# Optimization experiments

Measured on AMD Instinct MI355X. Metric: run time of the kernel, lower is better.

## Reference

```python
import jax, jax.numpy as jnp
import numpy as np

EPS = 1e-12

def setup_inputs() -> dict:
    key = jax.random.key(0)
    k1, k2, k3, k4, k5, k6 = jax.random.split(key, 6)
    B, DIM, T = 16, 256, 2048
    K, D = 1024, 64  # num_embeddings, embedding_dim
    N = B * T
    input_data = jax.random.normal(k1, (B, DIM, T), dtype=jnp.float32)
    codebooks = jax.random.normal(k2, (K, D), dtype=jnp.float32)
    W_in = jax.random.normal(k3, (DIM, D), dtype=jnp.float32) / np.sqrt(DIM)
    b_in = jnp.zeros((D,), dtype=jnp.float32)
    W_out = jax.random.normal(k4, (D, DIM), dtype=jnp.float32) / np.sqrt(D)
    b_out = jnp.zeros((DIM,), dtype=jnp.float32)
    random_vector = jax.random.normal(k5, (N, D), dtype=jnp.float32)
    return {"input_data": input_data, "codebooks": codebooks,
            "W_in": W_in, "b_in": b_in, "W_out": W_out, "b_out": b_out,
            "random_vector": random_vector}

def reference(input_data, codebooks, W_in, b_in, W_out, b_out, random_vector):
    B, DIM, T = input_data.shape
    D = codebooks.shape[1]
    # encode: [B, DIM, T] -> [B, T, DIM] -> project -> [B*T, D]
    x = jnp.einsum('bct,cd->btd', input_data, W_in) + b_in
    x = x.reshape(-1, D)  # [N, D]
    distances = (jnp.sum(x * x, axis=1, keepdims=True)
                 - 2.0 * (x @ codebooks.T)
                 + jnp.sum(codebooks * codebooks, axis=1)[None, :])  # [N, K]
    min_indices = jnp.argmin(distances, axis=1)  # [N]
    hard = codebooks[min_indices]  # [N, D]
    # noise substitution
    norm_resid = jnp.sqrt(jnp.sum((x - hard) ** 2, axis=1, keepdims=True))
    norm_rand = jnp.sqrt(jnp.sum(random_vector ** 2, axis=1, keepdims=True))
    vq_error = (norm_resid / (norm_rand + EPS)) * random_vector
    q = x + vq_error  # [N, D]
    # decode: [N, D] -> [B, T, D] -> project_out -> [B, DIM, T]
    q = q.reshape(B, T, D)
    out = jnp.einsum('btd,dc->bct', q, W_out) + b_out[None, :, None]
    return out
```

## Files before the change

kernel.cpp:

```cpp
#include <hip/hip_runtime.h>
#include <hip/hip_bf16.h>

typedef __bf16 bf16x8 __attribute__((ext_vector_type(8)));
typedef unsigned short u16x8 __attribute__((ext_vector_type(8)));
typedef unsigned int u32x2 __attribute__((ext_vector_type(2)));
typedef float f32x4 __attribute__((ext_vector_type(4)));
typedef unsigned short u16;

constexpr int DIMc = 256, Tt = 2048, Dd = 64;

#define CBF_U  0
#define CN_U   65536
#define WINT_U 67584
#define WOX_U  83968

__device__ __forceinline__ u16 f2b(float f) {
  unsigned u = __float_as_uint(f);
  return (u16)((u + 0x7FFFu + ((u >> 16) & 1u)) >> 16);
}
__device__ __forceinline__ float b2f(u16 v) {
  return __uint_as_float(((unsigned)v) << 16);
}
__device__ __forceinline__ unsigned f2b2(float a, float b) {
  return (unsigned)f2b(a) | ((unsigned)f2b(b) << 16);
}
__device__ __forceinline__ f32x4 mfma16(u16x8 a, u16x8 b, f32x4 c) {
  return __builtin_amdgcn_mfma_f32_16x16x32_bf16(
      __builtin_bit_cast(bf16x8, a), __builtin_bit_cast(bf16x8, b), c, 0, 0, 0);
}
__device__ __forceinline__ void dma16(const u16* g, u16* l) {
  __builtin_amdgcn_global_load_lds(
      (const __attribute__((address_space(1))) unsigned int*)g,
      (__attribute__((address_space(3))) unsigned int*)l, 16, 0, 0);
}

__global__ void nsvq_prep(const float* __restrict__ cb, const float* __restrict__ Win,
                          const float* __restrict__ Wout, u16* __restrict__ wsu) {
  const int g = blockIdx.x * 256 + threadIdx.x;
  {
    const int k = g >> 4, j = (g & 15) << 2;
    float4 v = *(const float4*)(cb + k * 64 + j);
    u16* row = wsu + CBF_U + k * 64 + j;
    row[0] = f2b(-2.f * v.x); row[1] = f2b(-2.f * v.y);
    row[2] = f2b(-2.f * v.z); row[3] = f2b(-2.f * v.w);
  }
  if (g < 1024) {
    const float* cr = cb + g * 64;
    float p[4];
    #pragma unroll
    for (int q = 0; q < 4; ++q) {
      float4 a0 = ((const float4*)(cr + q * 8))[0],      a1 = ((const float4*)(cr + q * 8))[1];
      float4 a2 = ((const float4*)(cr + 32 + q * 8))[0], a3 = ((const float4*)(cr + 32 + q * 8))[1];
      float pA = fmaf(a0.w, a0.w, fmaf(a0.z, a0.z, fmaf(a0.y, a0.y, a0.x * a0.x)));
      float pB = fmaf(a1.w, a1.w, fmaf(a1.z, a1.z, fmaf(a1.y, a1.y, a1.x * a1.x)));
      float pC = fmaf(a2.w, a2.w, fmaf(a2.z, a2.z, fmaf(a2.y, a2.y, a2.x * a2.x)));
      float pD = fmaf(a3.w, a3.w, fmaf(a3.z, a3.z, fmaf(a3.y, a3.y, a3.x * a3.x)));
      p[q] = (pA + pB) + (pC + pD);
    }
    ((float*)(wsu + CN_U))[g] = (p[0] + p[1]) + (p[2] + p[3]);
  }
  {
    const int d = g >> 8, c = g & 255;
    wsu[WINT_U + d * 256 + (((c >> 3) ^ (d & 7)) << 3) + (c & 7)] = f2b(Win[c * 64 + d]);
  }
  {
    const int c = g >> 6, d = g & 63;
    wsu[WOX_U + c * 64 + (((d >> 3) ^ (c & 7)) << 3) + (d & 7)] = f2b(Wout[d * 256 + c]);
  }
}

__global__ __launch_bounds__(256, 2) void nsvq_main(
    const float* __restrict__ in, const float* __restrict__ rnd,
    const float* __restrict__ bin, const float* __restrict__ bout,
    const u16* __restrict__ wsu, float* __restrict__ out) {
  __shared__ u16 sm[37376];
  u16* const WinT = sm;
  u16* const WoX  = sm + 16384;
  u16* const Xt   = sm + 32768;
  float* const mnp = (float*)(sm + 36864);

  const int tid  = threadIdx.x;
  const int lane = tid & 63;
  const int w    = tid >> 6;
  const int quad = lane >> 4, col = lane & 15;
  const int b    = blockIdx.x >> 5;
  const int t0   = (blockIdx.x & 31) << 6;
  const int myt  = w * 16 + col;

  #pragma unroll
  for (int ii = 0; ii < 8; ++ii) {
    const int i = w + 4 * ii;
    dma16(wsu + WINT_U + i * 512 + lane * 8, WinT + i * 512);
  }
  #pragma unroll
  for (int ii = 0; ii < 8; ++ii) {
    const int i = w + 4 * ii;
    dma16(wsu + WOX_U + i * 512 + lane * 8, WoX + i * 512);
  }
  u16x8 Bf[8];
  const float* ibase = in + (size_t)b * DIMc * Tt + t0 + myt;
  #pragma unroll
  for (int kt = 0; kt < 8; ++kt) {
    float v[8];
    #pragma unroll
    for (int j = 0; j < 8; ++j) v[j] = ibase[(size_t)(kt * 32 + quad * 8 + j) * Tt];
    u16x8 pk;
    #pragma unroll
    for (int j = 0; j < 8; ++j) pk[j] = f2b(v[j]);
    Bf[kt] = pk;
  }
  float4 rq[4];
  {
    const float* rbase = rnd + ((size_t)b * Tt + t0 + myt) * Dd + quad * 4;
    #pragma unroll
    for (int mt = 0; mt < 4; ++mt) rq[mt] = *(const float4*)(rbase + mt * 16);
  }
  float rr2v = 0.f;
  #pragma unroll
  for (int mt = 0; mt < 4; ++mt) {
    rr2v = fmaf(rq[mt].x, rq[mt].x, rr2v); rr2v = fmaf(rq[mt].y, rq[mt].y, rr2v);
    rr2v = fmaf(rq[mt].z, rq[mt].z, rr2v); rr2v = fmaf(rq[mt].w, rq[mt].w, rr2v);
  }
  rr2v += __shfl_xor(rr2v, 16);
  rr2v += __shfl_xor(rr2v, 32);
  __syncthreads();

  f32x4 acc[4];
  #pragma unroll
  for (int mt = 0; mt < 4; ++mt) {
    float4 bi = *(const float4*)(bin + mt * 16 + quad * 4);
    f32x4 a = {bi.x, bi.y, bi.z, bi.w};
    const int d = mt * 16 + col;
    #pragma unroll
    for (int kt = 0; kt < 8; ++kt) {
      u16x8 A = *(const u16x8*)(WinT + d * 256 + (((kt * 4 + quad) ^ (d & 7)) << 3));
      a = mfma16(A, Bf[kt], a);
    }
    acc[mt] = a;
  }
  float x2v = 0.f;
  #pragma unroll
  for (int mt = 0; mt < 4; ++mt) {
    #pragma unroll
    for (int r = 0; r < 4; ++r) x2v = fmaf(acc[mt][r], acc[mt][r], x2v);
    u32x2 px = { f2b2(acc[mt][0], acc[mt][1]), f2b2(acc[mt][2], acc[mt][3]) };
    const int bk  = mt * 2 + (quad >> 1);
    const int off = myt * 64 + ((bk ^ (myt & 7)) << 3) + (quad & 1) * 4;
    *(u32x2*)(Xt + off) = px;
  }
  x2v += __shfl_xor(x2v, 16);
  x2v += __shfl_xor(x2v, 32);
  __syncthreads();

  u16x8 Xa[4], Xb[4];
  #pragma unroll
  for (int nt = 0; nt < 4; ++nt) {
    const int tr = nt * 16 + col;
    Xa[nt] = *(const u16x8*)(Xt + tr * 64 + ((quad ^ (tr & 7)) << 3));
    Xb[nt] = *(const u16x8*)(Xt + tr * 64 + (((4 + quad) ^ (tr & 7)) << 3));
  }
  float minv[4];
  #pragma unroll
  for (int i = 0; i < 4; ++i) minv[i] = 3.4e38f;
  const u16* cwf   = wsu + CBF_U + (size_t)(w * 256) * 64;
  const float* cnp = (const float*)(wsu + CN_U) + w * 256;
  #pragma unroll 4
  for (int mi = 0; mi < 16; ++mi) {
    u16x8 A0 = *(const u16x8*)(cwf + (mi * 16 + col) * 64 + quad * 8);
    u16x8 A1 = *(const u16x8*)(cwf + (mi * 16 + col) * 64 + 32 + quad * 8);
    f32x4 cn4 = *(const f32x4*)(cnp + mi * 16 + quad * 4);
    #pragma unroll
    for (int nt = 0; nt < 4; ++nt) {
      f32x4 a = mfma16(A0, Xa[nt], cn4);
      a = mfma16(A1, Xb[nt], a);
      #pragma unroll
      for (int r = 0; r < 4; ++r) minv[nt] = fminf(minv[nt], a[r]);
    }
  }
  #pragma unroll
  for (int nt = 0; nt < 4; ++nt) {
    float m = minv[nt];
    m = fminf(m, __shfl_xor(m, 16));
    m = fminf(m, __shfl_xor(m, 32));
    mnp[w * 64 + nt * 16 + col] = m;
  }
  __syncthreads();

  float mv = 3.4e38f;
  #pragma unroll
  for (int j = 0; j < 4; ++j) mv = fminf(mv, mnp[j * 64 + myt]);
  float r2  = fmaxf(x2v + mv, 0.f);
  float scv = sqrtf(r2) / (sqrtf(rr2v) + 1e-12f);
  #pragma unroll
  for (int mt = 0; mt < 4; ++mt) {
    float q0 = fmaf(scv, rq[mt].x, acc[mt][0]);
    float q1 = fmaf(scv, rq[mt].y, acc[mt][1]);
    float q2 = fmaf(scv, rq[mt].z, acc[mt][2]);
    float q3 = fmaf(scv, rq[mt].w, acc[mt][3]);
    u32x2 pq = { f2b2(q0, q1), f2b2(q2, q3) };
    const int bk  = mt * 2 + (quad >> 1);
    const int off = myt * 64 + ((bk ^ (myt & 7)) << 3) + (quad & 1) * 4;
    *(u32x2*)(Xt + off) = pq;
  }

  u16x8 Q0 = *(const u16x8*)(Xt + myt * 64 + ((quad ^ (myt & 7)) << 3));
  u16x8 Q1 = *(const u16x8*)(Xt + myt * 64 + (((4 + quad) ^ (myt & 7)) << 3));
  float* ob0 = out + (size_t)b * DIMc * Tt + t0 + myt;
  #pragma unroll
  for (int mt = 0; mt < 16; ++mt) {
    const int c = mt * 16 + col;
    const u16* ar = WoX + c * 64;
    u16x8 A0 = *(const u16x8*)(ar + ((quad ^ (c & 7)) << 3));
    u16x8 A1 = *(const u16x8*)(ar + (((4 + quad) ^ (c & 7)) << 3));
    float4 bo = *(const float4*)(bout + mt * 16 + quad * 4);
    f32x4 a = {bo.x, bo.y, bo.z, bo.w};
    a = mfma16(A0, Q0, a);
    a = mfma16(A1, Q1, a);
    float* ob = ob0 + (size_t)(mt * 16 + quad * 4) * Tt;
    #pragma unroll
    for (int r = 0; r < 4; ++r) ob[(size_t)r * Tt] = a[r];
  }
}

extern "C" void kernel_launch(void* const* d_in, const int* in_sizes, int n_in,
                              void* d_out, int out_size, void* d_ws, size_t ws_size,
                              hipStream_t stream) {
  const float *in = nullptr, *cbp = nullptr, *rnd = nullptr, *bin = nullptr, *bout = nullptr;
  const float* w16[2] = {nullptr, nullptr}; int nw = 0;
  for (int i = 0; i < n_in; ++i) {
    switch (in_sizes[i]) {
      case 8388608: in  = (const float*)d_in[i]; break;
      case 65536:   cbp = (const float*)d_in[i]; break;
      case 2097152: rnd = (const float*)d_in[i]; break;
      case 64:      bin = (const float*)d_in[i]; break;
      case 256:     bout= (const float*)d_in[i]; break;
      case 16384:   if (nw < 2) w16[nw++] = (const float*)d_in[i]; break;
      default: break;
    }
  }
  if (!in)   in  = (const float*)d_in[0];
  if (!cbp)  cbp = (const float*)d_in[1];
  if (nw < 2) { w16[0] = (const float*)d_in[2]; w16[1] = (const float*)d_in[4]; }
  if (!bin)  bin = (const float*)d_in[3];
  if (!bout) bout = (const float*)d_in[5];
  if (!rnd)  rnd = (const float*)d_in[6];

  u16* wsu = (u16*)d_ws;
  nsvq_prep<<<64, 256, 0, stream>>>(cbp, w16[0], w16[1], wsu);
  nsvq_main<<<512, 256, 0, stream>>>(in, rnd, bin, bout, wsu, (float*)d_out);
}
```

Before: 113.0 us.

## Shrink blocks to 32 tokens, read weights from global, drop LDS weight staging

Each block now handles 32 tokens with 2 waves (1024 blocks of 128 threads) instead of 64 tokens with 4 waves. The W_in and W_out tiles are no longer copied into LDS; MFMA operands are read directly from global/L2 in an unswizzled layout. The random vector is reloaded instead of held in registers. This cuts LDS use and register pressure to allow more resident waves, at the cost of more global/L2 traffic for weights and codebook per token and twice the codebook scan per wave.

After: 132.5 us. 1.17x slower.

```diff
diff --git a/kernel.cpp b/kernel.cpp
--- a/kernel.cpp
+++ b/kernel.cpp
@@ -27,11 +27,6 @@
 __device__ __forceinline__ f32x4 mfma16(u16x8 a, u16x8 b, f32x4 c) {
   return __builtin_amdgcn_mfma_f32_16x16x32_bf16(
       __builtin_bit_cast(bf16x8, a), __builtin_bit_cast(bf16x8, b), c, 0, 0, 0);
-}
-__device__ __forceinline__ void dma16(const u16* g, u16* l) {
-  __builtin_amdgcn_global_load_lds(
-      (const __attribute__((address_space(1))) unsigned int*)g,
-      (__attribute__((address_space(3))) unsigned int*)l, 16, 0, 0);
 }
 
 __global__ void nsvq_prep(const float* __restrict__ cb, const float* __restrict__ Win,
@@ -61,42 +56,30 @@
   }
   {
     const int d = g >> 8, c = g & 255;
-    wsu[WINT_U + d * 256 + (((c >> 3) ^ (d & 7)) << 3) + (c & 7)] = f2b(Win[c * 64 + d]);
+    wsu[WINT_U + d * 256 + c] = f2b(Win[c * 64 + d]);
   }
   {
     const int c = g >> 6, d = g & 63;
-    wsu[WOX_U + c * 64 + (((d >> 3) ^ (c & 7)) << 3) + (d & 7)] = f2b(Wout[d * 256 + c]);
-  }
-}
-
-__global__ __launch_bounds__(256, 2) void nsvq_main(
+    wsu[WOX_U + c * 64 + d] = f2b(Wout[d * 256 + c]);
+  }
+}
+
+__global__ __launch_bounds__(128, 5) void nsvq_main(
     const float* __restrict__ in, const float* __restrict__ rnd,
     const float* __restrict__ bin, const float* __restrict__ bout,
     const u16* __restrict__ wsu, float* __restrict__ out) {
-  __shared__ u16 sm[37376];
-  u16* const WinT = sm;
-  u16* const WoX  = sm + 16384;
-  u16* const Xt   = sm + 32768;
-  float* const mnp = (float*)(sm + 36864);
+  __shared__ u16 sm[2176];
+  u16* const Xt   = sm;
+  float* const mnp = (float*)(sm + 2048);
 
   const int tid  = threadIdx.x;
   const int lane = tid & 63;
   const int w    = tid >> 6;
   const int quad = lane >> 4, col = lane & 15;
-  const int b    = blockIdx.x >> 5;
-  const int t0   = (blockIdx.x & 31) << 6;
+  const int b    = blockIdx.x >> 6;
+  const int t0   = (blockIdx.x & 63) << 5;
   const int myt  = w * 16 + col;
 
-  #pragma unroll
-  for (int ii = 0; ii < 8; ++ii) {
-    const int i = w + 4 * ii;
-    dma16(wsu + WINT_U + i * 512 + lane * 8, WinT + i * 512);
-  }
-  #pragma unroll
-  for (int ii = 0; ii < 8; ++ii) {
-    const int i = w + 4 * ii;
-    dma16(wsu + WOX_U + i * 512 + lane * 8, WoX + i * 512);
-  }
   u16x8 Bf[8];
   const float* ibase = in + (size_t)b * DIMc * Tt + t0 + myt;
   #pragma unroll
@@ -109,22 +92,18 @@
     for (int j = 0; j < 8; ++j) pk[j] = f2b(v[j]);
     Bf[kt] = pk;
   }
-  float4 rq[4];
-  {
-    const float* rbase = rnd + ((size_t)b * Tt + t0 + myt) * Dd + quad * 4;
-    #pragma unroll
-    for (int mt = 0; mt < 4; ++mt) rq[mt] = *(const float4*)(rbase + mt * 16);
-  }
+  const float* rbase = rnd + ((size_t)b * Tt + t0 + myt) * Dd + quad * 4;
   float rr2v = 0.f;
   #pragma unroll
   for (int mt = 0; mt < 4; ++mt) {
-    rr2v = fmaf(rq[mt].x, rq[mt].x, rr2v); rr2v = fmaf(rq[mt].y, rq[mt].y, rr2v);
-    rr2v = fmaf(rq[mt].z, rq[mt].z, rr2v); rr2v = fmaf(rq[mt].w, rq[mt].w, rr2v);
+    float4 r = *(const float4*)(rbase + mt * 16);
+    rr2v = fmaf(r.x, r.x, rr2v); rr2v = fmaf(r.y, r.y, rr2v);
+    rr2v = fmaf(r.z, r.z, rr2v); rr2v = fmaf(r.w, r.w, rr2v);
   }
   rr2v += __shfl_xor(rr2v, 16);
   rr2v += __shfl_xor(rr2v, 32);
-  __syncthreads();
-
+
+  const u16* wsWin = wsu + WINT_U;
   f32x4 acc[4];
   #pragma unroll
   for (int mt = 0; mt < 4; ++mt) {
@@ -133,7 +112,7 @@
     const int d = mt * 16 + col;
     #pragma unroll
     for (int kt = 0; kt < 8; ++kt) {
-      u16x8 A = *(const u16x8*)(WinT + d * 256 + (((kt * 4 + quad) ^ (d & 7)) << 3));
+      u16x8 A = *(const u16x8*)(wsWin + d * 256 + kt * 32 + quad * 8);
       a = mfma16(A, Bf[kt], a);
     }
     acc[mt] = a;
@@ -152,25 +131,23 @@
   x2v += __shfl_xor(x2v, 32);
   __syncthreads();
 
-  u16x8 Xa[4], Xb[4];
-  #pragma unroll
-  for (int nt = 0; nt < 4; ++nt) {
+  u16x8 Xa[2], Xb[2];
+  #pragma unroll
+  for (int nt = 0; nt < 2; ++nt) {
     const int tr = nt * 16 + col;
     Xa[nt] = *(const u16x8*)(Xt + tr * 64 + ((quad ^ (tr & 7)) << 3));
     Xb[nt] = *(const u16x8*)(Xt + tr * 64 + (((4 + quad) ^ (tr & 7)) << 3));
   }
-  float minv[4];
-  #pragma unroll
-  for (int i = 0; i < 4; ++i) minv[i] = 3.4e38f;
-  const u16* cwf   = wsu + CBF_U + (size_t)(w * 256) * 64;
-  const float* cnp = (const float*)(wsu + CN_U) + w * 256;
+  float minv[2] = {3.4e38f, 3.4e38f};
+  const u16* cwf   = wsu + CBF_U + (size_t)(w * 512) * 64;
+  const float* cnp = (const float*)(wsu + CN_U) + w * 512;
   #pragma unroll 4
-  for (int mi = 0; mi < 16; ++mi) {
+  for (int mi = 0; mi < 32; ++mi) {
     u16x8 A0 = *(const u16x8*)(cwf + (mi * 16 + col) * 64 + quad * 8);
     u16x8 A1 = *(const u16x8*)(cwf + (mi * 16 + col) * 64 + 32 + quad * 8);
     f32x4 cn4 = *(const f32x4*)(cnp + mi * 16 + quad * 4);
     #pragma unroll
-    for (int nt = 0; nt < 4; ++nt) {
+    for (int nt = 0; nt < 2; ++nt) {
       f32x4 a = mfma16(A0, Xa[nt], cn4);
       a = mfma16(A1, Xb[nt], a);
       #pragma unroll
@@ -178,25 +155,24 @@
     }
   }
   #pragma unroll
-  for (int nt = 0; nt < 4; ++nt) {
+  for (int nt = 0; nt < 2; ++nt) {
     float m = minv[nt];
     m = fminf(m, __shfl_xor(m, 16));
     m = fminf(m, __shfl_xor(m, 32));
-    mnp[w * 64 + nt * 16 + col] = m;
+    mnp[w * 32 + nt * 16 + col] = m;
   }
   __syncthreads();
 
-  float mv = 3.4e38f;
-  #pragma unroll
-  for (int j = 0; j < 4; ++j) mv = fminf(mv, mnp[j * 64 + myt]);
+  float mv = fminf(mnp[myt], mnp[32 + myt]);
   float r2  = fmaxf(x2v + mv, 0.f);
   float scv = sqrtf(r2) / (sqrtf(rr2v) + 1e-12f);
   #pragma unroll
   for (int mt = 0; mt < 4; ++mt) {
-    float q0 = fmaf(scv, rq[mt].x, acc[mt][0]);
-    float q1 = fmaf(scv, rq[mt].y, acc[mt][1]);
-    float q2 = fmaf(scv, rq[mt].z, acc[mt][2]);
-    float q3 = fmaf(scv, rq[mt].w, acc[mt][3]);
+    float4 r = *(const float4*)(rbase + mt * 16);
+    float q0 = fmaf(scv, r.x, acc[mt][0]);
+    float q1 = fmaf(scv, r.y, acc[mt][1]);
+    float q2 = fmaf(scv, r.z, acc[mt][2]);
+    float q3 = fmaf(scv, r.w, acc[mt][3]);
     u32x2 pq = { f2b2(q0, q1), f2b2(q2, q3) };
     const int bk  = mt * 2 + (quad >> 1);
     const int off = myt * 64 + ((bk ^ (myt & 7)) << 3) + (quad & 1) * 4;
@@ -205,13 +181,13 @@
 
   u16x8 Q0 = *(const u16x8*)(Xt + myt * 64 + ((quad ^ (myt & 7)) << 3));
   u16x8 Q1 = *(const u16x8*)(Xt + myt * 64 + (((4 + quad) ^ (myt & 7)) << 3));
+  const u16* wsWo = wsu + WOX_U;
   float* ob0 = out + (size_t)b * DIMc * Tt + t0 + myt;
   #pragma unroll
   for (int mt = 0; mt < 16; ++mt) {
     const int c = mt * 16 + col;
-    const u16* ar = WoX + c * 64;
-    u16x8 A0 = *(const u16x8*)(ar + ((quad ^ (c & 7)) << 3));
-    u16x8 A1 = *(const u16x8*)(ar + (((4 + quad) ^ (c & 7)) << 3));
+    u16x8 A0 = *(const u16x8*)(wsWo + c * 64 + quad * 8);
+    u16x8 A1 = *(const u16x8*)(wsWo + c * 64 + 32 + quad * 8);
     float4 bo = *(const float4*)(bout + mt * 16 + quad * 4);
     f32x4 a = {bo.x, bo.y, bo.z, bo.w};
     a = mfma16(A0, Q0, a);
@@ -247,5 +223,5 @@
 
   u16* wsu = (u16*)d_ws;
   nsvq_prep<<<64, 256, 0, stream>>>(cbp, w16[0], w16[1], wsu);
-  nsvq_main<<<512, 256, 0, stream>>>(in, rnd, bin, bout, wsu, (float*)d_out);
-}
+  nsvq_main<<<1024, 128, 0, stream>>>(in, rnd, bin, bout, wsu, (float*)d_out);
+}
```
